# Kernel optimization log

Measured on AMD Instinct MI355X. Metric: run time of the kernel, lower is better.

The kernel has to match this reference:

```python
import jax, jax.numpy as jnp
import numpy as np

IMG = 224
RADIUS_CUTS, AZIMUTH_CUTS = 16, 64
N_RADIUS, N_AZIMUTH = 25, 16          # kr1*kr2 = 25, ka^2 = 16
N_R = RADIUS_CUTS * N_RADIUS          # 400 sampled radii
N_A = AZIMUTH_CUTS * N_AZIMUTH        # 1024 sampled azimuths
EMBED_DIM = 96
KR, KA = 5, 4


def sample_grid(dist, H, W):
    """Per-batch polar sampling coordinates for the spherical distortion model.
    dist: (B, 4) polynomial distortion coefficients (module does dist.transpose(1,0)).
    Returns grid (B, N_R, N_A, 2) in grid_sample convention (x=width coord first),
    and theta_max (B,).
    """
    B = dist.shape[0]
    cf = 0.2 + dist.T                      # (4, B), positive odd-poly coefficients
    c = cf[:, :, None]                     # (4, B, 1) for broadcasting
    theta_max = jnp.full((B,), jnp.pi / 2, dtype=dist.dtype)

    def poly(t):                           # odd polynomial r(theta), t: (B, n)
        t2 = t * t
        return t * (c[0] + t2 * (c[1] + t2 * (c[2] + t2 * c[3])))

    # midpoint theta samples in (0, theta_max)
    theta = theta_max[:, None] * (jnp.arange(N_R, dtype=dist.dtype) + 0.5) / N_R  # (B, N_R)
    r = poly(theta) / poly(theta_max[:, None]) * (H * 0.5)                        # (B, N_R) pixels from center

    phi = (2.0 * jnp.pi) * (jnp.arange(N_A, dtype=dist.dtype) + 0.5) / N_A        # (N_A,)
    xc = r[:, :, None] * jnp.cos(phi)      # (B, N_R, N_A)
    yc = r[:, :, None] * jnp.sin(phi)
    # module: out = cat((yc/(W//2), xc/(H//2)), dim=3)
    grid = jnp.stack([yc / (W // 2), xc / (H // 2)], axis=-1)
    return grid, theta_max


def grid_sample_bilinear(img, grid):
    """torch.nn.functional.grid_sample, bilinear, align_corners=True, zeros padding.
    img: (B,C,H,W), grid: (B,Ho,Wo,2) with grid[...,0]=x (width), grid[...,1]=y (height).
    """
    B, C, H, W = img.shape
    gx = (grid[..., 0] + 1.0) * 0.5 * (W - 1)   # align_corners=True mapping
    gy = (grid[..., 1] + 1.0) * 0.5 * (H - 1)
    x0 = jnp.floor(gx); y0 = jnp.floor(gy)
    wx1 = gx - x0; wx0 = 1.0 - wx1
    wy1 = gy - y0; wy0 = 1.0 - wy1

    def corner(xi, yi, w):
        valid = (xi >= 0) & (xi <= W - 1) & (yi >= 0) & (yi <= H - 1)
        xc_ = jnp.clip(xi, 0, W - 1).astype(jnp.int32)
        yc_ = jnp.clip(yi, 0, H - 1).astype(jnp.int32)
        v = jax.vmap(lambda im, yy, xx: im[:, yy, xx])(img, yc_, xc_)  # (B,C,Ho,Wo)
        return v * (w * valid)[:, None, :, :]

    return (corner(x0, y0, wx0 * wy0) + corner(x0 + 1, y0, wx1 * wy0)
            + corner(x0, y0 + 1, wx0 * wy1) + corner(x0 + 1, y0 + 1, wx1 * wy1))


def conv2d(x, w, b, stride):
    y = jax.lax.conv_general_dilated(x, w, window_strides=stride, padding='VALID',
                                     dimension_numbers=('NCHW', 'OIHW', 'NCHW'))
    return y + b[None, :, None, None]


def setup_inputs() -> dict:
    key = jax.random.key(0)
    k = jax.random.split(key, 6)
    x = jax.random.uniform(k[0], (32, 3, IMG, IMG), dtype=jnp.float32)
    dist = jax.random.uniform(k[1], (32, 4), dtype=jnp.float32)
    w1 = jax.random.normal(k[2], (EMBED_DIM, 3, KR, KA), dtype=jnp.float32) * 0.05
    b1 = jnp.zeros((EMBED_DIM,), dtype=jnp.float32)
    w2 = jax.random.normal(k[3], (EMBED_DIM, EMBED_DIM, KR, KA), dtype=jnp.float32) * 0.05
    b2 = jnp.zeros((EMBED_DIM,), dtype=jnp.float32)
    return {"x": x, "dist": dist, "w1": w1, "b1": b1, "w2": w2, "b2": b2}


def reference(x, dist, w1, b1, w2, b2):
    B, C, H, W = x.shape
    grid, theta_max = sample_grid(dist, H, W)          # (B,400,1024,2)
    sampled = grid_sample_bilinear(x, grid)            # (B,3,400,1024)
    t = conv2d(sampled, w1, b1, (KR, KA))              # (B,96,80,256)
    t = conv2d(t, w2, b2, (KR, KA))                    # (B,96,16,64)
    t = t.reshape(B, EMBED_DIM, -1).transpose(0, 2, 1) # (B,1024,96)
    return (t, theta_max)
```

## Files before the change

### kernel.cpp

```cpp
#include <hip/hip_runtime.h>
#include <hip/hip_bf16.h>
#include <math.h>

#define NBATCH 32
#define IMGSZ  224
#define NR     400
#define NA     1024
#define ED     96
#define SROW   266

typedef __attribute__((ext_vector_type(8))) __bf16 bf16x8;
typedef __attribute__((ext_vector_type(8), aligned(8))) __bf16 bf16x8u;
typedef __attribute__((ext_vector_type(4), aligned(8))) __bf16 bf16x4a;
typedef __attribute__((ext_vector_type(4))) __bf16 bf16x4;
typedef __attribute__((ext_vector_type(4))) float f32x4;

union frag_u { struct { bf16x4a lo, hi; } p; bf16x8 v; };


#define PACK_N   (NBATCH*IMGSZ*IMGSZ)
#define PACK_N4  (PACK_N/4)
#define PACK_B   ((PACK_N4 + 255)/256)
#define PREP_N   (ED*ED*20 + 12*64*8 + NBATCH*NR + NA + NBATCH)
#define PREP_B   ((PREP_N + 255)/256)

__global__ __launch_bounds__(256)
void prep_pack_kernel(const float* __restrict__ x,
                      const float* __restrict__ dist,
                      const float* __restrict__ w1,
                      const float* __restrict__ w2,
                      __bf16* __restrict__ xp,
                      float* __restrict__ rtab,
                      float* __restrict__ costab,
                      float* __restrict__ sintab,
                      __bf16* __restrict__ w2f,
                      __bf16* __restrict__ w1f,
                      float* __restrict__ theta_out) {
    const float PI = 3.14159265358979323846f;
    const float SC = 223.0f / 224.0f;
    int bid = blockIdx.x;

    if (bid < PACK_B) {
        int i4 = bid*256 + threadIdx.x;
        if (i4 >= PACK_N4) return;
        int idx = i4 * 4;
        int b  = idx / (IMGSZ*IMGSZ);
        int px = idx - b*(IMGSZ*IMGSZ);
        const float* p = x + (size_t)b*3*IMGSZ*IMGSZ + px;
        f32x4 cr = *(const f32x4*)(p);
        f32x4 cg = *(const f32x4*)(p + IMGSZ*IMGSZ);
        f32x4 cb = *(const f32x4*)(p + 2*IMGSZ*IMGSZ);
        bf16x8 o0, o1;
        o0[0] = (__bf16)cr[0]; o0[1] = (__bf16)cg[0]; o0[2] = (__bf16)cb[0]; o0[3] = (__bf16)0.0f;
        o0[4] = (__bf16)cr[1]; o0[5] = (__bf16)cg[1]; o0[6] = (__bf16)cb[1]; o0[7] = (__bf16)0.0f;
        o1[0] = (__bf16)cr[2]; o1[1] = (__bf16)cg[2]; o1[2] = (__bf16)cb[2]; o1[3] = (__bf16)0.0f;
        o1[4] = (__bf16)cr[3]; o1[5] = (__bf16)cg[3]; o1[6] = (__bf16)cb[3]; o1[7] = (__bf16)0.0f;
        *(bf16x8*)(xp + (size_t)idx*4)     = o0;
        *(bf16x8*)(xp + (size_t)idx*4 + 8) = o1;
        return;
    }

    int idx = (bid - PACK_B)*256 + threadIdx.x;
    if (idx < ED*ED*20) {
        int j    = idx & 7;
        int lane = (idx >> 3) & 63;
        int grp  = idx >> 9;
        int nt   = grp % 6;
        int t    = grp / 6;
        int icb  = t % 3;
        int p    = t / 3;
        int sw   = (((p & 3) + icb) & 1) * 4;
        int oc = nt*16 + (lane & 15);
        int ic = icb*32 + (lane >> 4)*8 + (j ^ sw);
        w2f[idx] = (__bf16)w2[((size_t)(oc*ED + ic)*5 + (p >> 2))*4 + (p & 3)];
    } else if (idx < ED*ED*20 + 12*64*8) {
        int i2   = idx - ED*ED*20;
        int j    = i2 & 7;
        int lane = (i2 >> 3) & 63;
        int grp  = i2 >> 9;
        int ks = grp / 6, ot = grp % 6;
        int oc = ot*16 + (lane & 15);
        int k  = ks*32 + (lane >> 4)*8 + j;
        w1f[i2] = (k < 60) ? (__bf16)w1[oc*60 + k] : (__bf16)0.0f;
    } else if (idx < ED*ED*20 + 12*64*8 + NBATCH*NR) {
        int i2 = idx - ED*ED*20 - 12*64*8;
        int b = i2 / NR, i = i2 % NR;
        float c0 = 0.2f + dist[b*4+0];
        float c1 = 0.2f + dist[b*4+1];
        float c2 = 0.2f + dist[b*4+2];
        float c3 = 0.2f + dist[b*4+3];
        float tmax = 0.5f * PI;
        float t  = tmax * ((float)i + 0.5f) / (float)NR;
        float t2 = t * t;
        float pt = t * (c0 + t2*(c1 + t2*(c2 + t2*c3)));
        float tm2 = tmax * tmax;
        float pm = tmax * (c0 + tm2*(c1 + tm2*(c2 + tm2*c3)));
        rtab[i2] = pt / pm * (0.5f * (float)IMGSZ);
    } else if (idx < ED*ED*20 + 12*64*8 + NBATCH*NR + NA) {
        int j = idx - ED*ED*20 - 12*64*8 - NBATCH*NR;
        float phi = 2.0f * PI * ((float)j + 0.5f) / (float)NA;
        costab[j] = cosf(phi) * SC;
        sintab[j] = sinf(phi) * SC;
    } else if (idx < PREP_N) {
        theta_out[idx - (ED*ED*20 + 12*64*8 + NBATCH*NR + NA)] = 0.5f * PI;
    }
}

__global__ __launch_bounds__(256, 5)
void mega_kernel(const __bf16* __restrict__ xp,
                 const __bf16* __restrict__ w1f_g,
                 const __bf16* __restrict__ w2f,
                 const float* __restrict__ b1,
                 const float* __restrict__ b2,
                 const float* __restrict__ rtab,
                 const float* __restrict__ costab,
                 const float* __restrict__ sintab,
                 float* __restrict__ out) {
    __shared__ __attribute__((aligned(16))) char smem[32576];
    __bf16* s_samp = (__bf16*)smem;
    __bf16* t1f    = (__bf16*)(smem + 8000);
    __bf16* s_w1f  = (__bf16*)(smem + 20288);
    float*  red    = (float*)smem;

    int tid = threadIdx.x;
    int bid = blockIdx.x;
    int r2 = bid & 15;
    int aq = (bid >> 4) & 3;
    int b  = bid >> 6;
    int wave = tid >> 6, lane = tid & 63, l15 = lane & 15, quad = lane >> 4;

    #pragma unroll
    for (int i = 0; i < 3; ++i)
        *(bf16x8*)(s_w1f + i*2048 + tid*8) = *(const bf16x8*)(w1f_g + i*2048 + tid*8);

    int az = aq*256 + tid;
    float sn = sintab[az];
    float cs = costab[az];
    const __bf16* xpb = xp + (size_t)b*IMGSZ*IMGSZ*4;
    const float* rb = rtab + b*NR + r2*25;

    f32x4 acc2[6];
    #pragma unroll
    for (int nt = 0; nt < 6; ++nt) acc2[nt] = (f32x4){0.f,0.f,0.f,0.f};

    auto sample = [&](int kr) {
        #pragma unroll
        for (int q = 0; q < 5; ++q) {
            float r  = rb[kr*5 + q];
            float gx = fmaf(r, sn, 111.5f);
            float gy = fmaf(r, cs, 111.5f);
            float x0f = floorf(gx), y0f = floorf(gy);
            float wx1 = gx - x0f, wx0 = 1.0f - wx1;
            float wy1 = gy - y0f, wy0 = 1.0f - wy1;
            int ix = (int)x0f, iy = (int)y0f;
            ix = min(max(ix, 0), IMGSZ-2);
            iy = min(max(iy, 0), IMGSZ-2);
            const __bf16* img = xpb + ((size_t)iy*IMGSZ + ix)*4;
            bf16x8u p0 = *(const bf16x8u*)img;
            bf16x8u p1 = *(const bf16x8u*)(img + IMGSZ*4);
            float w00 = wy0*wx0, w01 = wy0*wx1, w10 = wy1*wx0, w11 = wy1*wx1;
            #pragma unroll
            for (int c = 0; c < 3; ++c) {
                float v = w00*(float)p0[c] + w01*(float)p0[4+c]
                        + w10*(float)p1[c] + w11*(float)p1[4+c];
                s_samp[(c*5 + q)*SROW + tid] = (__bf16)v;
            }
        }
    };

    sample(0);

    for (int kr = 0; kr < 5; ++kr) {
        __syncthreads();

        int colb = (wave*16 + l15)*4;
        f32x4 acc1[6];
        #pragma unroll
        for (int ot = 0; ot < 6; ++ot) acc1[ot] = (f32x4){0.f,0.f,0.f,0.f};

        frag_u fa, fb;
        fa.p.lo = *(const bf16x4a*)&s_samp[(quad*2    )*SROW + colb];
        fa.p.hi = *(const bf16x4a*)&s_samp[(quad*2 + 1)*SROW + colb];
        fb.p.lo = *(const bf16x4a*)&s_samp[(8 + quad*2)*SROW + colb];
        if (quad == 3) fb.p.hi = (bf16x4a){};
        else           fb.p.hi = *(const bf16x4a*)&s_samp[(9 + quad*2)*SROW + colb];

        #pragma unroll
        for (int ot = 0; ot < 6; ++ot) {
            bf16x8 wf0 = *(const bf16x8*)(s_w1f + (ot     )*512 + lane*8);
            bf16x8 wf1 = *(const bf16x8*)(s_w1f + (6 + ot )*512 + lane*8);
            acc1[ot] = __builtin_amdgcn_mfma_f32_16x16x32_bf16(wf0, fa.v, acc1[ot], 0, 0, 0);
            acc1[ot] = __builtin_amdgcn_mfma_f32_16x16x32_bf16(wf1, fb.v, acc1[ot], 0, 0, 0);
        }

        int pixel = wave*16 + l15;
        int a2l = pixel >> 2, ka = pixel & 3;
        #pragma unroll
        for (int ot = 0; ot < 6; ++ot) {
            f32x4 v = acc1[ot] + *(const f32x4*)(b1 + ot*16 + quad*4);
            bf16x4a wv;
            wv[0] = (__bf16)v[0]; wv[1] = (__bf16)v[1];
            wv[2] = (__bf16)v[2]; wv[3] = (__bf16)v[3];
            int icbase = ot*16 + quad*4;
            int kk = ka*3 + (icbase >> 5);
            int qT = (icbase >> 3) & 3;
            int jb = (icbase & 7) ^ ((kk & 1)*4);
            *(bf16x4a*)&t1f[((kk*4 + qT)*16 + a2l)*8 + jb] = wv;
        }
        __syncthreads();

        #pragma unroll
        for (int icb = 0; icb < 3; ++icb) {
            int kk = wave*3 + icb;
            int p  = kr*4 + wave;
            bf16x8 af = *(const bf16x8*)&t1f[(kk*64 + lane)*8];
            const __bf16* wp = w2f + (size_t)((p*3 + icb)*6)*512 + lane*8;
            #pragma unroll
            for (int nt = 0; nt < 6; ++nt) {
                bf16x8 bf = *(const bf16x8*)(wp + nt*512);
                acc2[nt] = __builtin_amdgcn_mfma_f32_16x16x32_bf16(af, bf, acc2[nt], 0, 0, 0);
            }
        }

        __builtin_amdgcn_sched_barrier(0);

        if (kr < 4) sample(kr + 1);
    }

    __syncthreads();
    if (wave) {
        float* rw = red + (wave - 1)*1568;
        #pragma unroll
        for (int nt = 0; nt < 6; ++nt)
            #pragma unroll
            for (int r = 0; r < 4; ++r)
                rw[(quad*4 + r)*98 + nt*16 + l15] = acc2[nt][r];
    }
    __syncthreads();
    if (wave == 0) {
        size_t ob = ((size_t)b*1024 + r2*64 + aq*16)*ED;
        #pragma unroll
        for (int nt = 0; nt < 6; ++nt) {
            int oc = nt*16 + l15;
            float bias = b2[oc];
            #pragma unroll
            for (int r = 0; r < 4; ++r) {
                int row = quad*4 + r;
                float v = acc2[nt][r] + bias
                        + red[row*98 + oc]
                        + red[1568 + row*98 + oc]
                        + red[3136 + row*98 + oc];
                out[ob + (size_t)row*ED + oc] = v;
            }
        }
    }
}

extern "C" void kernel_launch(void* const* d_in, const int* in_sizes, int n_in,
                              void* d_out, int out_size, void* d_ws, size_t ws_size,
                              hipStream_t stream) {
    const float* x    = (const float*)d_in[0];
    const float* dist = (const float*)d_in[1];
    const float* w1   = (const float*)d_in[2];
    const float* b1   = (const float*)d_in[3];
    const float* w2   = (const float*)d_in[4];
    const float* b2   = (const float*)d_in[5];
    float* out = (float*)d_out;

    float* rtab   = (float*)d_ws;
    float* costab = rtab + NBATCH*NR;
    float* sintab = costab + NA;
    __bf16* w2f   = (__bf16*)(sintab + NA);
    __bf16* w1f   = w2f + ED*ED*20;
    __bf16* xp    = w1f + 12*64*8;

    float* theta_out = out + (size_t)NBATCH*1024*ED;

    prep_pack_kernel<<<PACK_B + PREP_B, 256, 0, stream>>>(
        x, dist, w1, w2, xp, rtab, costab, sintab, w2f, w1f, theta_out);
    mega_kernel<<<NBATCH*16*4, 256, 0, stream>>>(
        xp, w1f, w2f, b1, b2, rtab, costab, sintab, out);
}
```

Before: 157.3 us.

## Make sampling and conv1 wave-local with double-buffered samples to drop block barriers

The azimuth-to-thread mapping is remapped so each wave samples exactly the pixel columns it later consumes in conv1, and writes only the t1f slices it reads for conv2. That makes every per-iteration stage wave-private, so both __syncthreads inside the kr loop are removed. The sample buffer is double-buffered so the next row can be produced while the current one is still being read. In exchange, shared memory grows and the launch-bounds occupancy hint drops from 5 to 4 blocks per CU, and the sample row stride loses its bank-conflict padding.

```diff
diff --git a/kernel.cpp b/kernel.cpp
--- a/kernel.cpp
+++ b/kernel.cpp
@@ -7,7 +7,7 @@
 #define NR     400
 #define NA     1024
 #define ED     96
-#define SROW   266
+#define SROW   256
 
 typedef __attribute__((ext_vector_type(8))) __bf16 bf16x8;
 typedef __attribute__((ext_vector_type(8), aligned(8))) __bf16 bf16x8u;
@@ -106,7 +106,7 @@
     }
 }
 
-__global__ __launch_bounds__(256, 5)
+__global__ __launch_bounds__(256, 4)
 void mega_kernel(const __bf16* __restrict__ xp,
                  const __bf16* __restrict__ w1f_g,
                  const __bf16* __restrict__ w2f,
@@ -116,11 +116,12 @@
                  const float* __restrict__ costab,
                  const float* __restrict__ sintab,
                  float* __restrict__ out) {
-    __shared__ __attribute__((aligned(16))) char smem[32576];
-    __bf16* s_samp = (__bf16*)smem;
-    __bf16* t1f    = (__bf16*)(smem + 8000);
-    __bf16* s_w1f  = (__bf16*)(smem + 20288);
-    float*  red    = (float*)smem;
+    __shared__ __attribute__((aligned(16))) char smem[39936];
+    __bf16* s_samp0 = (__bf16*)smem;
+    __bf16* s_samp1 = (__bf16*)(smem + 7680);
+    __bf16* t1f     = (__bf16*)(smem + 15360);
+    __bf16* s_w1f   = (__bf16*)(smem + 27648);
+    float*  red     = (float*)smem;
 
     int tid = threadIdx.x;
     int bid = blockIdx.x;
@@ -133,9 +134,11 @@
     for (int i = 0; i < 3; ++i)
         *(bf16x8*)(s_w1f + i*2048 + tid*8) = *(const bf16x8*)(w1f_g + i*2048 + tid*8);
 
-    int az = aq*256 + tid;
+    int col = ((lane >> 2) << 4) + wave*4 + (lane & 3);
+    int az  = aq*256 + col;
     float sn = sintab[az];
     float cs = costab[az];
+    int scol = wave*64 + lane;
     const __bf16* xpb = xp + (size_t)b*IMGSZ*IMGSZ*4;
     const float* rb = rtab + b*NR + r2*25;
 
@@ -143,7 +146,7 @@
     #pragma unroll
     for (int nt = 0; nt < 6; ++nt) acc2[nt] = (f32x4){0.f,0.f,0.f,0.f};
 
-    auto sample = [&](int kr) {
+    auto sample = [&](int kr, __bf16* sb) {
         #pragma unroll
         for (int q = 0; q < 5; ++q) {
             float r  = rb[kr*5 + q];
@@ -163,27 +166,28 @@
             for (int c = 0; c < 3; ++c) {
                 float v = w00*(float)p0[c] + w01*(float)p0[4+c]
                         + w10*(float)p1[c] + w11*(float)p1[4+c];
-                s_samp[(c*5 + q)*SROW + tid] = (__bf16)v;
+                sb[(c*5 + q)*SROW + scol] = (__bf16)v;
             }
         }
     };
 
-    sample(0);
+    sample(0, s_samp0);
+    __syncthreads();
 
     for (int kr = 0; kr < 5; ++kr) {
-        __syncthreads();
-
-        int colb = (wave*16 + l15)*4;
+        __bf16* sb = (kr & 1) ? s_samp1 : s_samp0;
+
+        int cb = wave*64 + l15*4;
         f32x4 acc1[6];
         #pragma unroll
         for (int ot = 0; ot < 6; ++ot) acc1[ot] = (f32x4){0.f,0.f,0.f,0.f};
 
         frag_u fa, fb;
-        fa.p.lo = *(const bf16x4a*)&s_samp[(quad*2    )*SROW + colb];
-        fa.p.hi = *(const bf16x4a*)&s_samp[(quad*2 + 1)*SROW + colb];
-        fb.p.lo = *(const bf16x4a*)&s_samp[(8 + quad*2)*SROW + colb];
+        fa.p.lo = *(const bf16x4a*)&sb[(quad*2    )*SROW + cb];
+        fa.p.hi = *(const bf16x4a*)&sb[(quad*2 + 1)*SROW + cb];
+        fb.p.lo = *(const bf16x4a*)&sb[(8 + quad*2)*SROW + cb];
         if (quad == 3) fb.p.hi = (bf16x4a){};
-        else           fb.p.hi = *(const bf16x4a*)&s_samp[(9 + quad*2)*SROW + colb];
+        else           fb.p.hi = *(const bf16x4a*)&sb[(9 + quad*2)*SROW + cb];
 
         #pragma unroll
         for (int ot = 0; ot < 6; ++ot) {
@@ -193,8 +197,6 @@
             acc1[ot] = __builtin_amdgcn_mfma_f32_16x16x32_bf16(wf1, fb.v, acc1[ot], 0, 0, 0);
         }
 
-        int pixel = wave*16 + l15;
-        int a2l = pixel >> 2, ka = pixel & 3;
         #pragma unroll
         for (int ot = 0; ot < 6; ++ot) {
             f32x4 v = acc1[ot] + *(const f32x4*)(b1 + ot*16 + quad*4);
@@ -202,12 +204,11 @@
             wv[0] = (__bf16)v[0]; wv[1] = (__bf16)v[1];
             wv[2] = (__bf16)v[2]; wv[3] = (__bf16)v[3];
             int icbase = ot*16 + quad*4;
-            int kk = ka*3 + (icbase >> 5);
+            int kk = wave*3 + (icbase >> 5);
             int qT = (icbase >> 3) & 3;
             int jb = (icbase & 7) ^ ((kk & 1)*4);
-            *(bf16x4a*)&t1f[((kk*4 + qT)*16 + a2l)*8 + jb] = wv;
-        }
-        __syncthreads();
+            *(bf16x4a*)&t1f[((kk*4 + qT)*16 + l15)*8 + jb] = wv;
+        }
 
         #pragma unroll
         for (int icb = 0; icb < 3; ++icb) {
@@ -224,7 +225,7 @@
 
         __builtin_amdgcn_sched_barrier(0);
 
-        if (kr < 4) sample(kr + 1);
+        if (kr < 4) sample(kr + 1, (kr & 1) ? s_samp0 : s_samp1);
     }
 
     __syncthreads();
```

Measured after the change: 140.5 us, median of 2. 1.12x faster.
